# Optimization experiments

Hardware: AMD Instinct MI355X
Metric: run time of the kernel (lower is better)

## Reference

```python
import jax, jax.numpy as jnp
import numpy as np

DIM = 1024
HEADS = 16
DIM_K = DIM // HEADS
B, S = 2, 2048


def setup_inputs() -> dict:
    key = jax.random.key(0)
    ks = jax.random.split(key, 8)
    scale = 1.0 / np.sqrt(DIM)
    Q = jax.random.normal(ks[0], (B, S, DIM), dtype=jnp.float32)
    K = jax.random.normal(ks[1], (B, S, DIM), dtype=jnp.float32)
    V = jax.random.normal(ks[2], (B, S, DIM), dtype=jnp.float32)
    # causal mask, broadcastable [1,1,S,S]; masked_fill where mask == 0
    mask = jnp.tril(jnp.ones((S, S), dtype=bool))[None, None, :, :]
    wq = jax.random.normal(ks[3], (DIM, DIM), dtype=jnp.float32) * scale
    wk = jax.random.normal(ks[4], (DIM, DIM), dtype=jnp.float32) * scale
    wv = jax.random.normal(ks[5], (DIM, DIM), dtype=jnp.float32) * scale
    wo_w = jax.random.normal(ks[6], (DIM, DIM), dtype=jnp.float32) * scale
    wo_b = jnp.zeros((DIM,), dtype=jnp.float32)
    return {"Q": Q, "K": K, "V": V, "mask": mask,
            "wq": wq, "wk": wk, "wv": wv, "wo_w": wo_w, "wo_b": wo_b}


def reference(Q, K, V, mask, wq, wk, wv, wo_w, wo_b):
    b, s, d = Q.shape
    n_k = K.shape[1]
    # nn.Linear(bias=False): x @ W^T
    q = (Q @ wq.T).reshape(b, s, HEADS, DIM_K).transpose(0, 2, 1, 3)    # [b,h,s,dk]
    k = (K @ wk.T).reshape(b, n_k, HEADS, DIM_K).transpose(0, 2, 1, 3)  # [b,h,nk,dk]
    v = (V @ wv.T).reshape(b, n_k, HEADS, DIM_K).transpose(0, 2, 1, 3)
    inv_sqrt_dk = 1.0 / np.sqrt(DIM_K).astype(np.float32)
    scores = jnp.einsum('bhsd,bhtd->bhst', q, k) * inv_sqrt_dk          # [b,h,s,nk]
    scores = jnp.where(mask, scores, jnp.float32(-1e9))
    weights = jax.nn.softmax(scores, axis=-1)  # dropout p=0 -> identity
    out = jnp.einsum('bhst,bhtd->bhsd', weights, v)
    out = out.transpose(0, 2, 1, 3).reshape(b, s, d)
    return out @ wo_w.T + wo_b
```

## Files before the change

kernel.cpp:

```cpp
#include <hip/hip_runtime.h>

#define DIMN 1024
#define HEADS 16
#define DK 64
#define BATCH 2
#define SEQ 2048
#define MROWS (BATCH*SEQ)

typedef __bf16 bf16x8 __attribute__((ext_vector_type(8)));
typedef float f32x4 __attribute__((ext_vector_type(4)));

__device__ __forceinline__ unsigned short f2bf(float f) {
    unsigned int u = __float_as_uint(f);
    u += 0x7FFFu + ((u >> 16) & 1u);
    return (unsigned short)(u >> 16);
}

__device__ __forceinline__ f32x4 mfma16(bf16x8 a, bf16x8 b, f32x4 c) {
    return __builtin_amdgcn_mfma_f32_16x16x32_bf16(a, b, c, 0, 0, 0);
}

__device__ __forceinline__ void gload_lds16(const void* g, void* l) {
    __builtin_amdgcn_global_load_lds(
        (const __attribute__((address_space(1))) unsigned int*)g,
        (__attribute__((address_space(3))) unsigned int*)l, 16, 0, 0);
}

__device__ __forceinline__ unsigned cvtpk_bf16(float lo, float hi) {
    unsigned r;
    asm("v_cvt_pk_bf16_f32 %0, %1, %2" : "=v"(r) : "v"(lo), "v"(hi));
    return r;
}

__global__ __launch_bounds__(256) void cvt_all_kernel(
    const float* __restrict__ s0, const float* __restrict__ s1, const float* __restrict__ s2,
    const float* __restrict__ s3, const float* __restrict__ s4, const float* __restrict__ s5,
    const float* __restrict__ s6,
    unsigned short* __restrict__ d0, unsigned short* __restrict__ d1,
    unsigned short* __restrict__ d2, unsigned short* __restrict__ d3,
    unsigned short* __restrict__ d4, unsigned short* __restrict__ d5,
    unsigned short* __restrict__ d6) {
    int bb = blockIdx.x;
    const float* src; unsigned short* dst; int base;
    if (bb < 12288) {
        int w = bb >> 12; base = bb & 4095;
        src = (w == 0) ? s0 : (w == 1) ? s1 : s2;
        dst = (w == 0) ? d0 : (w == 1) ? d1 : d2;
    } else {
        int w = (bb - 12288) >> 10; base = bb & 1023;
        src = (w == 0) ? s3 : (w == 1) ? s4 : (w == 2) ? s5 : s6;
        dst = (w == 0) ? d3 : (w == 1) ? d4 : (w == 2) ? d5 : d6;
    }
    int i = (base * 256 + threadIdx.x) * 4;
    float4 v = *reinterpret_cast<const float4*>(src + i);
    ushort4 o;
    o.x = f2bf(v.x); o.y = f2bf(v.y); o.z = f2bf(v.z); o.w = f2bf(v.w);
    *reinterpret_cast<ushort4*>(dst + i) = o;
}

template<int BMM, bool OUT_F32, bool BIAS, typename CT>
__device__ __forceinline__ void gemm_core(
    const unsigned short* __restrict__ A, const unsigned short* __restrict__ W,
    CT* __restrict__ Cv, const float* __restrict__ bias, float oscale,
    unsigned short (&Asm)[2][BMM * 32], unsigned short (&Bsm)[2][128 * 32]) {
    const int tid = threadIdx.x, wid = tid >> 6, lane = tid & 63;
    const int m0 = blockIdx.x * BMM, n0 = blockIdx.y * 128;
    constexpr int MR = BMM / 32;
    const int wr = (wid >> 1) * (BMM / 2), wc = (wid & 1) * 64;
    const int lrow = lane & 15, lko = (lane >> 4) * 8;

    f32x4 acc[MR][4];
#pragma unroll
    for (int m = 0; m < MR; m++)
#pragma unroll
        for (int n = 0; n < 4; n++) acc[m][n] = f32x4{0.f, 0.f, 0.f, 0.f};

    const int offA = wid * 1024 + lane * 16;
    auto stage = [&](int buf, int k0) {
#pragma unroll
        for (int j = 0; j < BMM / 64; j++) {
            int off = j * 4096 + offA;
            int row = off >> 6, colb = off & 63;
            gload_lds16(A + (size_t)(m0 + row) * DIMN + k0 + (colb >> 1),
                        &Asm[buf][(j * 4096 + wid * 1024) >> 1]);
        }
#pragma unroll
        for (int j = 0; j < 2; j++) {
            int off = j * 4096 + offA;
            int row = off >> 6, colb = off & 63;
            gload_lds16(W + (size_t)(n0 + row) * DIMN + k0 + (colb >> 1),
                        &Bsm[buf][(j * 4096 + wid * 1024) >> 1]);
        }
    };

    stage(0, 0);
    __syncthreads();
    const int nk = DIMN / 32;
    int cur = 0;
    for (int t = 0; t < nk; t++) {
        if (t + 1 < nk) stage(cur ^ 1, (t + 1) * 32);
        bf16x8 af[MR], bfr[4];
#pragma unroll
        for (int m = 0; m < MR; m++)
            af[m] = *(const bf16x8*)&Asm[cur][(wr + m * 16 + lrow) * 32 + lko];
#pragma unroll
        for (int n = 0; n < 4; n++)
            bfr[n] = *(const bf16x8*)&Bsm[cur][(wc + n * 16 + lrow) * 32 + lko];
#pragma unroll
        for (int m = 0; m < MR; m++)
#pragma unroll
            for (int n = 0; n < 4; n++)
                acc[m][n] = mfma16(af[m], bfr[n], acc[m][n]);
        __syncthreads();
        cur ^= 1;
    }

    const int rbase = (lane >> 4) * 4;
    const int cbase = lane & 15;
#pragma unroll
    for (int m = 0; m < MR; m++) {
#pragma unroll
        for (int n = 0; n < 4; n++) {
#pragma unroll
            for (int r = 0; r < 4; r++) {
                int row = m0 + wr + m * 16 + rbase + r;
                int col = n0 + wc + n * 16 + cbase;
                float v = acc[m][n][r] * oscale;
                if (BIAS) v += bias[col];
                if (OUT_F32)
                    ((float*)Cv)[(size_t)row * DIMN + col] = v;
                else
                    ((unsigned short*)Cv)[(size_t)row * DIMN + col] = f2bf(v);
            }
        }
    }
}

__global__ __launch_bounds__(256, 2) void gemm_proj3_kernel(
    const unsigned short* __restrict__ A0, const unsigned short* __restrict__ A1,
    const unsigned short* __restrict__ A2,
    const unsigned short* __restrict__ W0, const unsigned short* __restrict__ W1,
    const unsigned short* __restrict__ W2,
    unsigned short* __restrict__ C0, unsigned short* __restrict__ C1,
    unsigned short* __restrict__ C2) {
    __shared__ unsigned short Asm[2][128 * 32];
    __shared__ unsigned short Bsm[2][128 * 32];
    const int z = blockIdx.z;
    const unsigned short* A = (z == 0) ? A0 : (z == 1) ? A1 : A2;
    const unsigned short* W = (z == 0) ? W0 : (z == 1) ? W1 : W2;
    unsigned short* C = (z == 0) ? C0 : (z == 1) ? C1 : C2;
    const float os = (z == 0) ? 0.18033688011112042f : 1.0f;
    gemm_core<128, false, false>(A, W, C, (const float*)nullptr, os, Asm, Bsm);
}

__global__ __launch_bounds__(256, 2) void gemm_out_kernel(
    const unsigned short* __restrict__ A, const unsigned short* __restrict__ W,
    float* __restrict__ C, const float* __restrict__ bias) {
    __shared__ unsigned short Asm[2][64 * 32];
    __shared__ unsigned short Bsm[2][128 * 32];
    gemm_core<64, true, true>(A, W, C, bias, 1.0f, Asm, Bsm);
}

__global__ __launch_bounds__(256) void vtrans_kernel(
    const unsigned short* __restrict__ vp, unsigned short* __restrict__ vt) {
    const int r0 = blockIdx.x * 64;
    const int h = blockIdx.y;
    const int b = r0 >> 11;
    const int s0 = r0 & 2047;
    __shared__ unsigned short T[64][72];
    const int tid = threadIdx.x;
#pragma unroll
    for (int jj = 0; jj < 2; jj++) {
        int idx = tid + 256 * jj;
        int row = idx >> 3, ch = idx & 7;
        uint4 v = *(const uint4*)(vp + (size_t)(r0 + row) * DIMN + h * DK + ch * 8);
        *(uint4*)&T[row][ch * 8] = v;
    }
    __syncthreads();
#pragma unroll
    for (int jj = 0; jj < 4; jj++) {
        int cid = tid + 256 * jj;
        int d = cid >> 4, rem = cid & 15;
        int G = rem >> 3, g = (rem >> 1) & 3, t = rem & 1;
        int sl = G * 32 + 16 * t + 4 * g;
        ushort4 o;
        o.x = T[sl + 0][d]; o.y = T[sl + 1][d]; o.z = T[sl + 2][d]; o.w = T[sl + 3][d];
        size_t orow = (size_t)((b * HEADS + h) * 64 + d);
        *(ushort4*)(vt + orow * SEQ + s0 + G * 32 + g * 8 + t * 4) = o;
    }
}

template<bool DIAG>
__device__ __forceinline__ void attn_tile(
    const unsigned short* __restrict__ Kc, const unsigned short* __restrict__ Vc,
    bf16x8 qf0, bf16x8 qf1, f32x4 (&o)[4], float& lrun,
    const int c, const int g, const int k0, const int qq) {
    float p[16];
    float rs = 0.f;
#pragma unroll
    for (int t = 0; t < 4; t++) {
        const int row = t * 16 + c;
        bf16x8 ka0 = *(const bf16x8*)&Kc[row * 64 + ((g ^ (c & 7)) * 8)];
        bf16x8 ka1 = *(const bf16x8*)&Kc[row * 64 + (((4 + g) ^ (c & 7)) * 8)];
        f32x4 s = mfma16(ka0, qf0, f32x4{0.f, 0.f, 0.f, 0.f});
        s = mfma16(ka1, qf1, s);
        const int kbase = k0 + t * 16 + 4 * g;
#pragma unroll
        for (int r = 0; r < 4; r++) {
            float pe = __builtin_exp2f(s[r]);
            if (DIAG && (kbase + r) > qq) pe = 0.f;
            p[t * 4 + r] = pe;
            rs += pe;
        }
    }
    rs += __shfl_xor(rs, 16);
    rs += __shfl_xor(rs, 32);
    lrun += rs;

    unsigned pk[8];
#pragma unroll
    for (int t = 0; t < 4; t++) {
        pk[t * 2 + 0] = cvtpk_bf16(p[t * 4 + 0], p[t * 4 + 1]);
        pk[t * 2 + 1] = cvtpk_bf16(p[t * 4 + 2], p[t * 4 + 3]);
    }
#pragma unroll
    for (int ks = 0; ks < 2; ks++) {
        union { unsigned u[4]; bf16x8 v; } pa;
        pa.u[0] = pk[4 * ks + 0]; pa.u[1] = pk[4 * ks + 1];
        pa.u[2] = pk[4 * ks + 2]; pa.u[3] = pk[4 * ks + 3];
#pragma unroll
        for (int dt = 0; dt < 4; dt++) {
            const int row = dt * 16 + c;
            bf16x8 vb = *(const bf16x8*)&Vc[row * 64 + ((((ks * 4) + g) ^ (c & 7)) * 8)];
            o[dt] = mfma16(pa.v, vb, o[dt]);
        }
    }
}

__global__ __launch_bounds__(256, 2) void attn_kernel(
    const unsigned short* __restrict__ qp, const unsigned short* __restrict__ kp,
    const unsigned short* __restrict__ vt, unsigned short* __restrict__ ao) {
    const int tid = threadIdx.x, wid = tid >> 6, lane = tid & 63;
    const int c = lane & 15, g = lane >> 4;
    const int blk = blockIdx.x;
    const int kk = blk >> 3;
    const int bh = (blk & 7) + 8 * (kk >> 4);
    const int j = kk & 15;
    const int qA = j * 64;
    const int qB = (31 - j) * 64;
    const int b = bh >> 4, h = bh & 15;

    __shared__ unsigned short Kt[2][64 * 64];
    __shared__ unsigned short Vt[2][64 * 64];

    const unsigned short* qrowA = qp + (size_t)(b * SEQ + qA + wid * 16 + c) * DIMN + h * DK;
    bf16x8 qfA0 = *(const bf16x8*)(qrowA + g * 8);
    bf16x8 qfA1 = *(const bf16x8*)(qrowA + 32 + g * 8);
    const unsigned short* qrowB = qp + (size_t)(b * SEQ + qB + wid * 16 + c) * DIMN + h * DK;
    bf16x8 qfB0 = *(const bf16x8*)(qrowB + g * 8);
    bf16x8 qfB1 = *(const bf16x8*)(qrowB + 32 + g * 8);

    f32x4 oA[4], oB[4];
#pragma unroll
    for (int dt = 0; dt < 4; dt++) {
        oA[dt] = f32x4{0.f, 0.f, 0.f, 0.f};
        oB[dt] = f32x4{0.f, 0.f, 0.f, 0.f};
    }
    float lrunA = 0.f, lrunB = 0.f;

    const int nktB = 32 - j;
    const int qqA = qA + wid * 16 + c;
    const int qqB = qB + wid * 16 + c;

    auto stage = [&](int buf, int k0) {
#pragma unroll
        for (int jj = 0; jj < 2; jj++) {
            int boff = (jj * 4 + wid) * 1024;
            int off = boff + lane * 16;
            int row = off >> 7;
            int sch = ((off >> 4) & 7) ^ (row & 7);
            gload_lds16(kp + (size_t)(b * SEQ + k0 + row) * DIMN + h * DK + sch * 8,
                        (char*)&Kt[buf][0] + boff);
            gload_lds16(vt + (size_t)(bh * 64 + row) * SEQ + k0 + sch * 8,
                        (char*)&Vt[buf][0] + boff);
        }
    };

    stage(0, 0);
    __syncthreads();
    int cur = 0;
    for (int kt = 0; kt < nktB; kt++) {
        if (kt + 1 < nktB) stage(cur ^ 1, (kt + 1) * 64);
        const int k0 = kt * 64;
        const unsigned short* Kc = &Kt[cur][0];
        const unsigned short* Vc = &Vt[cur][0];

        if (kt == nktB - 1)
            attn_tile<true>(Kc, Vc, qfB0, qfB1, oB, lrunB, c, g, k0, qqB);
        else
            attn_tile<false>(Kc, Vc, qfB0, qfB1, oB, lrunB, c, g, k0, qqB);

        if (kt < j)
            attn_tile<false>(Kc, Vc, qfA0, qfA1, oA, lrunA, c, g, k0, qqA);
        else if (kt == j)
            attn_tile<true>(Kc, Vc, qfA0, qfA1, oA, lrunA, c, g, k0, qqA);

        __syncthreads();
        cur ^= 1;
    }

    float lrA[4], lrB[4];
#pragma unroll
    for (int r = 0; r < 4; r++) {
        lrA[r] = 1.0f / __shfl(lrunA, 4 * g + r);
        lrB[r] = 1.0f / __shfl(lrunB, 4 * g + r);
    }
#pragma unroll
    for (int dt = 0; dt < 4; dt++)
#pragma unroll
        for (int r = 0; r < 4; r++) {
            ao[(size_t)(b * SEQ + qA + wid * 16 + 4 * g + r) * DIMN + h * DK + dt * 16 + c] =
                f2bf(oA[dt][r] * lrA[r]);
            ao[(size_t)(b * SEQ + qB + wid * 16 + 4 * g + r) * DIMN + h * DK + dt * 16 + c] =
                f2bf(oB[dt][r] * lrB[r]);
        }
}

extern "C" void kernel_launch(void* const* d_in, const int* in_sizes, int n_in,
                              void* d_out, int out_size, void* d_ws, size_t ws_size,
                              hipStream_t stream) {
    const float* Q  = (const float*)d_in[0];
    const float* K  = (const float*)d_in[1];
    const float* V  = (const float*)d_in[2];
    const float* wq = (const float*)d_in[4];
    const float* wk = (const float*)d_in[5];
    const float* wv = (const float*)d_in[6];
    const float* wo = (const float*)d_in[7];
    const float* wob = (const float*)d_in[8];

    char* ws = (char*)d_ws;
    const size_t SZ_ACT = (size_t)MROWS * DIMN * 2;
    const size_t SZ_W   = (size_t)DIMN * DIMN * 2;
    unsigned short* Qb  = (unsigned short*)(ws);
    unsigned short* Kb  = (unsigned short*)(ws + SZ_ACT);
    unsigned short* Vb  = (unsigned short*)(ws + 2 * SZ_ACT);
    unsigned short* Wqb = (unsigned short*)(ws + 3 * SZ_ACT);
    unsigned short* Wkb = (unsigned short*)(ws + 3 * SZ_ACT + SZ_W);
    unsigned short* Wvb = (unsigned short*)(ws + 3 * SZ_ACT + 2 * SZ_W);
    unsigned short* Wob = (unsigned short*)(ws + 3 * SZ_ACT + 3 * SZ_W);
    unsigned short* qp  = (unsigned short*)(ws + 3 * SZ_ACT + 4 * SZ_W);
    unsigned short* kp  = (unsigned short*)(ws + 4 * SZ_ACT + 4 * SZ_W);
    unsigned short* vp  = (unsigned short*)(ws + 5 * SZ_ACT + 4 * SZ_W);
    unsigned short* vt  = Vb;
    unsigned short* aob = Qb;

    cvt_all_kernel<<<16384, 256, 0, stream>>>(Q, K, V, wq, wk, wv, wo,
                                              Qb, Kb, Vb, Wqb, Wkb, Wvb, Wob);

    dim3 gp(MROWS / 128, DIMN / 128, 3);
    gemm_proj3_kernel<<<gp, 256, 0, stream>>>(Qb, Kb, Vb, Wqb, Wkb, Wvb, qp, kp, vp);

    dim3 gt(MROWS / 64, HEADS);
    vtrans_kernel<<<gt, 256, 0, stream>>>(vp, vt);

    attn_kernel<<<512, 256, 0, stream>>>(qp, kp, vt, aob);

    dim3 go(MROWS / 64, DIMN / 128);
    gemm_out_kernel<<<go, 256, 0, stream>>>(aob, Wob, (float*)d_out, wob);
}
```

Measured before the change: 133.7 us.

## Fuse fp32-to-bf16 activation conversion into projection GEMM and swizzle LDS tiles

The Q/K/V inputs are no longer converted to bf16 in a separate pass. The projection GEMM now loads fp32 tiles straight into LDS and converts them to bf16 with v_cvt_pk_bf16_f32 just before the MFMA. This removes a full read and write of the 48 MB of activations, though the GEMM now pulls twice the A bytes per tile and uses more LDS. XOR swizzling is also added to the LDS layouts of A and B to cut bank conflicts on fragment reads.

```diff
diff --git a/kernel.cpp b/kernel.cpp
--- a/kernel.cpp
+++ b/kernel.cpp
@@ -32,25 +32,15 @@
     return r;
 }
 
-__global__ __launch_bounds__(256) void cvt_all_kernel(
-    const float* __restrict__ s0, const float* __restrict__ s1, const float* __restrict__ s2,
-    const float* __restrict__ s3, const float* __restrict__ s4, const float* __restrict__ s5,
-    const float* __restrict__ s6,
+__global__ __launch_bounds__(256) void cvt_w_kernel(
+    const float* __restrict__ s0, const float* __restrict__ s1,
+    const float* __restrict__ s2, const float* __restrict__ s3,
     unsigned short* __restrict__ d0, unsigned short* __restrict__ d1,
-    unsigned short* __restrict__ d2, unsigned short* __restrict__ d3,
-    unsigned short* __restrict__ d4, unsigned short* __restrict__ d5,
-    unsigned short* __restrict__ d6) {
+    unsigned short* __restrict__ d2, unsigned short* __restrict__ d3) {
     int bb = blockIdx.x;
-    const float* src; unsigned short* dst; int base;
-    if (bb < 12288) {
-        int w = bb >> 12; base = bb & 4095;
-        src = (w == 0) ? s0 : (w == 1) ? s1 : s2;
-        dst = (w == 0) ? d0 : (w == 1) ? d1 : d2;
-    } else {
-        int w = (bb - 12288) >> 10; base = bb & 1023;
-        src = (w == 0) ? s3 : (w == 1) ? s4 : (w == 2) ? s5 : s6;
-        dst = (w == 0) ? d3 : (w == 1) ? d4 : (w == 2) ? d5 : d6;
-    }
+    int w = bb >> 10, base = bb & 1023;
+    const float* src = (w == 0) ? s0 : (w == 1) ? s1 : (w == 2) ? s2 : s3;
+    unsigned short* dst = (w == 0) ? d0 : (w == 1) ? d1 : (w == 2) ? d2 : d3;
     int i = (base * 256 + threadIdx.x) * 4;
     float4 v = *reinterpret_cast<const float4*>(src + i);
     ushort4 o;
@@ -58,16 +48,16 @@
     *reinterpret_cast<ushort4*>(dst + i) = o;
 }
 
-template<int BMM, bool OUT_F32, bool BIAS, typename CT>
+template<int BMM, bool AF32, bool OUT_F32, bool BIAS>
 __device__ __forceinline__ void gemm_core(
-    const unsigned short* __restrict__ A, const unsigned short* __restrict__ W,
-    CT* __restrict__ Cv, const float* __restrict__ bias, float oscale,
-    unsigned short (&Asm)[2][BMM * 32], unsigned short (&Bsm)[2][128 * 32]) {
+    const void* __restrict__ Av, const unsigned short* __restrict__ W,
+    void* __restrict__ Cv, const float* __restrict__ bias, float oscale,
+    void* __restrict__ AsmV, unsigned short (&Bsm)[2][128 * 32]) {
     const int tid = threadIdx.x, wid = tid >> 6, lane = tid & 63;
     const int m0 = blockIdx.x * BMM, n0 = blockIdx.y * 128;
     constexpr int MR = BMM / 32;
     const int wr = (wid >> 1) * (BMM / 2), wc = (wid & 1) * 64;
-    const int lrow = lane & 15, lko = (lane >> 4) * 8;
+    const int lrow = lane & 15, g = lane >> 4;
 
     f32x4 acc[MR][4];
 #pragma unroll
@@ -75,37 +65,74 @@
 #pragma unroll
         for (int n = 0; n < 4; n++) acc[m][n] = f32x4{0.f, 0.f, 0.f, 0.f};
 
-    const int offA = wid * 1024 + lane * 16;
-    auto stage = [&](int buf, int k0) {
-#pragma unroll
-        for (int j = 0; j < BMM / 64; j++) {
-            int off = j * 4096 + offA;
-            int row = off >> 6, colb = off & 63;
-            gload_lds16(A + (size_t)(m0 + row) * DIMN + k0 + (colb >> 1),
-                        &Asm[buf][(j * 4096 + wid * 1024) >> 1]);
-        }
-#pragma unroll
-        for (int j = 0; j < 2; j++) {
-            int off = j * 4096 + offA;
-            int row = off >> 6, colb = off & 63;
-            gload_lds16(W + (size_t)(n0 + row) * DIMN + k0 + (colb >> 1),
-                        &Bsm[buf][(j * 4096 + wid * 1024) >> 1]);
+    auto stageA = [&](int buf, int k0) {
+        if constexpr (AF32) {
+            const float* Af = (const float*)Av;
+#pragma unroll
+            for (int jj = 0; jj < BMM / 32; jj++) {
+                int off = jj * 4096 + wid * 1024 + lane * 16;
+                int row = off >> 7;
+                int sch = ((off >> 4) & 7) ^ (row & 7);
+                gload_lds16(Af + (size_t)(m0 + row) * DIMN + k0 + sch * 4,
+                            (char*)AsmV + buf * (BMM * 128) + jj * 4096 + wid * 1024);
+            }
+        } else {
+            const unsigned short* Ab = (const unsigned short*)Av;
+#pragma unroll
+            for (int jj = 0; jj < BMM / 64; jj++) {
+                int off = jj * 4096 + wid * 1024 + lane * 16;
+                int row = off >> 6;
+                int sch = ((off >> 4) & 3) ^ ((row >> 1) & 3);
+                gload_lds16(Ab + (size_t)(m0 + row) * DIMN + k0 + sch * 8,
+                            (char*)AsmV + buf * (BMM * 64) + jj * 4096 + wid * 1024);
+            }
         }
     };
-
-    stage(0, 0);
+    auto stageB = [&](int buf, int k0) {
+#pragma unroll
+        for (int jj = 0; jj < 2; jj++) {
+            int off = jj * 4096 + wid * 1024 + lane * 16;
+            int row = off >> 6;
+            int sch = ((off >> 4) & 3) ^ ((row >> 1) & 3);
+            gload_lds16(W + (size_t)(n0 + row) * DIMN + k0 + sch * 8,
+                        (char*)&Bsm[buf][0] + jj * 4096 + wid * 1024);
+        }
+    };
+
+    stageA(0, 0); stageB(0, 0);
     __syncthreads();
-    const int nk = DIMN / 32;
     int cur = 0;
-    for (int t = 0; t < nk; t++) {
-        if (t + 1 < nk) stage(cur ^ 1, (t + 1) * 32);
+    for (int t = 0; t < 32; t++) {
+        if (t + 1 < 32) { stageA(cur ^ 1, (t + 1) * 32); stageB(cur ^ 1, (t + 1) * 32); }
         bf16x8 af[MR], bfr[4];
-#pragma unroll
-        for (int m = 0; m < MR; m++)
-            af[m] = *(const bf16x8*)&Asm[cur][(wr + m * 16 + lrow) * 32 + lko];
-#pragma unroll
-        for (int n = 0; n < 4; n++)
-            bfr[n] = *(const bf16x8*)&Bsm[cur][(wc + n * 16 + lrow) * 32 + lko];
+        if constexpr (AF32) {
+            const float* Asm = (const float*)AsmV + cur * (BMM * 32);
+#pragma unroll
+            for (int m = 0; m < MR; m++) {
+                int row = wr + m * 16 + lrow;
+                int c0 = (2 * g) ^ (row & 7), c1 = (2 * g + 1) ^ (row & 7);
+                f32x4 lo = *(const f32x4*)&Asm[row * 32 + c0 * 4];
+                f32x4 hi = *(const f32x4*)&Asm[row * 32 + c1 * 4];
+                union { unsigned u[4]; bf16x8 v; } a;
+                a.u[0] = cvtpk_bf16(lo[0], lo[1]); a.u[1] = cvtpk_bf16(lo[2], lo[3]);
+                a.u[2] = cvtpk_bf16(hi[0], hi[1]); a.u[3] = cvtpk_bf16(hi[2], hi[3]);
+                af[m] = a.v;
+            }
+        } else {
+            const unsigned short* Asm = (const unsigned short*)AsmV + cur * (BMM * 32);
+#pragma unroll
+            for (int m = 0; m < MR; m++) {
+                int row = wr + m * 16 + lrow;
+                int ch = g ^ ((row >> 1) & 3);
+                af[m] = *(const bf16x8*)&Asm[row * 32 + ch * 8];
+            }
+        }
+#pragma unroll
+        for (int n = 0; n < 4; n++) {
+            int row = wc + n * 16 + lrow;
+            int ch = g ^ ((row >> 1) & 3);
+            bfr[n] = *(const bf16x8*)&Bsm[cur][row * 32 + ch * 8];
+        }
 #pragma unroll
         for (int m = 0; m < MR; m++)
 #pragma unroll
@@ -115,8 +142,7 @@
         cur ^= 1;
     }
 
-    const int rbase = (lane >> 4) * 4;
-    const int cbase = lane & 15;
+    const int rbase = g * 4;
 #pragma unroll
     for (int m = 0; m < MR; m++) {
 #pragma unroll
@@ -124,7 +150,7 @@
 #pragma unroll
             for (int r = 0; r < 4; r++) {
                 int row = m0 + wr + m * 16 + rbase + r;
-                int col = n0 + wc + n * 16 + cbase;
+                int col = n0 + wc + n * 16 + lrow;
                 float v = acc[m][n][r] * oscale;
                 if (BIAS) v += bias[col];
                 if (OUT_F32)
@@ -137,28 +163,28 @@
 }
 
 __global__ __launch_bounds__(256, 2) void gemm_proj3_kernel(
-    const unsigned short* __restrict__ A0, const unsigned short* __restrict__ A1,
-    const unsigned short* __restrict__ A2,
+    const float* __restrict__ A0, const float* __restrict__ A1,
+    const float* __restrict__ A2,
     const unsigned short* __restrict__ W0, const unsigned short* __restrict__ W1,
     const unsigned short* __restrict__ W2,
     unsigned short* __restrict__ C0, unsigned short* __restrict__ C1,
     unsigned short* __restrict__ C2) {
-    __shared__ unsigned short Asm[2][128 * 32];
+    __shared__ float AsmF[2][128 * 32];
     __shared__ unsigned short Bsm[2][128 * 32];
     const int z = blockIdx.z;
-    const unsigned short* A = (z == 0) ? A0 : (z == 1) ? A1 : A2;
+    const float* A = (z == 0) ? A0 : (z == 1) ? A1 : A2;
     const unsigned short* W = (z == 0) ? W0 : (z == 1) ? W1 : W2;
     unsigned short* C = (z == 0) ? C0 : (z == 1) ? C1 : C2;
     const float os = (z == 0) ? 0.18033688011112042f : 1.0f;
-    gemm_core<128, false, false>(A, W, C, (const float*)nullptr, os, Asm, Bsm);
+    gemm_core<128, true, false, false>(A, W, C, (const float*)nullptr, os, AsmF, Bsm);
 }
 
 __global__ __launch_bounds__(256, 2) void gemm_out_kernel(
     const unsigned short* __restrict__ A, const unsigned short* __restrict__ W,
     float* __restrict__ C, const float* __restrict__ bias) {
-    __shared__ unsigned short Asm[2][64 * 32];
+    __shared__ unsigned short AsmH[2][64 * 32];
     __shared__ unsigned short Bsm[2][128 * 32];
-    gemm_core<64, true, true>(A, W, C, bias, 1.0f, Asm, Bsm);
+    gemm_core<64, false, true, true>(A, W, C, bias, 1.0f, AsmH, Bsm);
 }
 
 __global__ __launch_bounds__(256) void vtrans_kernel(
@@ -341,29 +367,25 @@
     char* ws = (char*)d_ws;
     const size_t SZ_ACT = (size_t)MROWS * DIMN * 2;
     const size_t SZ_W   = (size_t)DIMN * DIMN * 2;
-    unsigned short* Qb  = (unsigned short*)(ws);
-    unsigned short* Kb  = (unsigned short*)(ws + SZ_ACT);
-    unsigned short* Vb  = (unsigned short*)(ws + 2 * SZ_ACT);
-    unsigned short* Wqb = (unsigned short*)(ws + 3 * SZ_ACT);
-    unsigned short* Wkb = (unsigned short*)(ws + 3 * SZ_ACT + SZ_W);
-    unsigned short* Wvb = (unsigned short*)(ws + 3 * SZ_ACT + 2 * SZ_W);
-    unsigned short* Wob = (unsigned short*)(ws + 3 * SZ_ACT + 3 * SZ_W);
-    unsigned short* qp  = (unsigned short*)(ws + 3 * SZ_ACT + 4 * SZ_W);
-    unsigned short* kp  = (unsigned short*)(ws + 4 * SZ_ACT + 4 * SZ_W);
-    unsigned short* vp  = (unsigned short*)(ws + 5 * SZ_ACT + 4 * SZ_W);
-    unsigned short* vt  = Vb;
-    unsigned short* aob = Qb;
-
-    cvt_all_kernel<<<16384, 256, 0, stream>>>(Q, K, V, wq, wk, wv, wo,
-                                              Qb, Kb, Vb, Wqb, Wkb, Wvb, Wob);
+    unsigned short* vtb = (unsigned short*)(ws);
+    unsigned short* aob = (unsigned short*)(ws + SZ_ACT);
+    unsigned short* Wqb = (unsigned short*)(ws + 2 * SZ_ACT);
+    unsigned short* Wkb = (unsigned short*)(ws + 2 * SZ_ACT + SZ_W);
+    unsigned short* Wvb = (unsigned short*)(ws + 2 * SZ_ACT + 2 * SZ_W);
+    unsigned short* Wob = (unsigned short*)(ws + 2 * SZ_ACT + 3 * SZ_W);
+    unsigned short* qp  = (unsigned short*)(ws + 2 * SZ_ACT + 4 * SZ_W);
+    unsigned short* kp  = (unsigned short*)(ws + 3 * SZ_ACT + 4 * SZ_W);
+    unsigned short* vp  = (unsigned short*)(ws + 4 * SZ_ACT + 4 * SZ_W);
+
+    cvt_w_kernel<<<4096, 256, 0, stream>>>(wq, wk, wv, wo, Wqb, Wkb, Wvb, Wob);
 
     dim3 gp(MROWS / 128, DIMN / 128, 3);
-    gemm_proj3_kernel<<<gp, 256, 0, stream>>>(Qb, Kb, Vb, Wqb, Wkb, Wvb, qp, kp, vp);
+    gemm_proj3_kernel<<<gp, 256, 0, stream>>>(Q, K, V, Wqb, Wkb, Wvb, qp, kp, vp);
 
     dim3 gt(MROWS / 64, HEADS);
-    vtrans_kernel<<<gt, 256, 0, stream>>>(vp, vt);
-
-    attn_kernel<<<512, 256, 0, stream>>>(qp, kp, vt, aob);
+    vtrans_kernel<<<gt, 256, 0, stream>>>(vp, vtb);
+
+    attn_kernel<<<512, 256, 0, stream>>>(qp, kp, vtb, aob);
 
     dim3 go(MROWS / 64, DIMN / 128);
     gemm_out_kernel<<<go, 256, 0, stream>>>(aob, Wob, (float*)d_out, wob);
```

After: 123.9 us. 7.4% less time.

## Swizzle GEMM LDS tiles, use explicit vmcnt waits, triple-buffer attention K/V

Applied to the files above, without the earlier changes.

The GEMM core now writes A and W tiles to LDS with an XOR swizzle on 16-byte chunks and reads them back with the matching swizzle, to avoid LDS bank conflicts on the fragment reads. Its loop replaces __syncthreads with explicit s_waitcnt vmcnt counts and raw s_barrier, so the next tile's async loads stay in flight while the current tile is computed. The attention kernel moves to a 3-stage K/V ring with a prefetch distance of two, and the projection GEMM's launch bounds go from 2 to 3 blocks. The hand-written vmcnt values assume a fixed number of outstanding loads per stage, so a wrong count could cause a race. The extra attention buffer also raises LDS use per block.

```diff
diff --git a/kernel.cpp b/kernel.cpp
--- a/kernel.cpp
+++ b/kernel.cpp
@@ -58,16 +58,16 @@
     *reinterpret_cast<ushort4*>(dst + i) = o;
 }
 
-template<int BMM, bool OUT_F32, bool BIAS, typename CT>
+template<int BMM, bool OUT_F32, bool BIAS>
 __device__ __forceinline__ void gemm_core(
     const unsigned short* __restrict__ A, const unsigned short* __restrict__ W,
-    CT* __restrict__ Cv, const float* __restrict__ bias, float oscale,
+    void* __restrict__ Cv, const float* __restrict__ bias, float oscale,
     unsigned short (&Asm)[2][BMM * 32], unsigned short (&Bsm)[2][128 * 32]) {
     const int tid = threadIdx.x, wid = tid >> 6, lane = tid & 63;
     const int m0 = blockIdx.x * BMM, n0 = blockIdx.y * 128;
     constexpr int MR = BMM / 32;
     const int wr = (wid >> 1) * (BMM / 2), wc = (wid & 1) * 64;
-    const int lrow = lane & 15, lko = (lane >> 4) * 8;
+    const int lrow = lane & 15, g = lane >> 4;
 
     f32x4 acc[MR][4];
 #pragma unroll
@@ -75,48 +75,67 @@
 #pragma unroll
         for (int n = 0; n < 4; n++) acc[m][n] = f32x4{0.f, 0.f, 0.f, 0.f};
 
-    const int offA = wid * 1024 + lane * 16;
-    auto stage = [&](int buf, int k0) {
-#pragma unroll
-        for (int j = 0; j < BMM / 64; j++) {
-            int off = j * 4096 + offA;
-            int row = off >> 6, colb = off & 63;
-            gload_lds16(A + (size_t)(m0 + row) * DIMN + k0 + (colb >> 1),
-                        &Asm[buf][(j * 4096 + wid * 1024) >> 1]);
-        }
-#pragma unroll
-        for (int j = 0; j < 2; j++) {
-            int off = j * 4096 + offA;
-            int row = off >> 6, colb = off & 63;
-            gload_lds16(W + (size_t)(n0 + row) * DIMN + k0 + (colb >> 1),
-                        &Bsm[buf][(j * 4096 + wid * 1024) >> 1]);
+    auto stageA = [&](int buf, int k0) {
+#pragma unroll
+        for (int jj = 0; jj < BMM / 64; jj++) {
+            int off = jj * 4096 + wid * 1024 + lane * 16;
+            int row = off >> 6;
+            int sch = ((off >> 4) & 3) ^ ((row >> 1) & 3);
+            gload_lds16(A + (size_t)(m0 + row) * DIMN + k0 + sch * 8,
+                        (char*)&Asm[buf][0] + jj * 4096 + wid * 1024);
         }
     };
-
-    stage(0, 0);
-    __syncthreads();
-    const int nk = DIMN / 32;
+    auto stageB = [&](int buf, int k0) {
+#pragma unroll
+        for (int jj = 0; jj < 2; jj++) {
+            int off = jj * 4096 + wid * 1024 + lane * 16;
+            int row = off >> 6;
+            int sch = ((off >> 4) & 3) ^ ((row >> 1) & 3);
+            gload_lds16(W + (size_t)(n0 + row) * DIMN + k0 + sch * 8,
+                        (char*)&Bsm[buf][0] + jj * 4096 + wid * 1024);
+        }
+    };
+
+    stageA(0, 0); stageB(0, 0);
     int cur = 0;
-    for (int t = 0; t < nk; t++) {
-        if (t + 1 < nk) stage(cur ^ 1, (t + 1) * 32);
+    for (int t = 0; t < 32; t++) {
+        if (t + 1 < 32) {
+            stageA(cur ^ 1, (t + 1) * 32); stageB(cur ^ 1, (t + 1) * 32);
+            if constexpr ((BMM / 64 + 2) == 3)
+                asm volatile("s_waitcnt vmcnt(3)" ::: "memory");
+            else
+                asm volatile("s_waitcnt vmcnt(4)" ::: "memory");
+        } else {
+            asm volatile("s_waitcnt vmcnt(0)" ::: "memory");
+        }
+        __builtin_amdgcn_s_barrier();
+        __builtin_amdgcn_sched_barrier(0);
+
         bf16x8 af[MR], bfr[4];
 #pragma unroll
-        for (int m = 0; m < MR; m++)
-            af[m] = *(const bf16x8*)&Asm[cur][(wr + m * 16 + lrow) * 32 + lko];
-#pragma unroll
-        for (int n = 0; n < 4; n++)
-            bfr[n] = *(const bf16x8*)&Bsm[cur][(wc + n * 16 + lrow) * 32 + lko];
+        for (int m = 0; m < MR; m++) {
+            int row = wr + m * 16 + lrow;
+            int ch = g ^ ((row >> 1) & 3);
+            af[m] = *(const bf16x8*)&Asm[cur][row * 32 + ch * 8];
+        }
+#pragma unroll
+        for (int n = 0; n < 4; n++) {
+            int row = wc + n * 16 + lrow;
+            int ch = g ^ ((row >> 1) & 3);
+            bfr[n] = *(const bf16x8*)&Bsm[cur][row * 32 + ch * 8];
+        }
 #pragma unroll
         for (int m = 0; m < MR; m++)
 #pragma unroll
             for (int n = 0; n < 4; n++)
                 acc[m][n] = mfma16(af[m], bfr[n], acc[m][n]);
-        __syncthreads();
+
+        __builtin_amdgcn_sched_barrier(0);
+        __builtin_amdgcn_s_barrier();
         cur ^= 1;
     }
 
-    const int rbase = (lane >> 4) * 4;
-    const int cbase = lane & 15;
+    const int rbase = g * 4;
 #pragma unroll
     for (int m = 0; m < MR; m++) {
 #pragma unroll
@@ -124,7 +143,7 @@
 #pragma unroll
             for (int r = 0; r < 4; r++) {
                 int row = m0 + wr + m * 16 + rbase + r;
-                int col = n0 + wc + n * 16 + cbase;
+                int col = n0 + wc + n * 16 + lrow;
                 float v = acc[m][n][r] * oscale;
                 if (BIAS) v += bias[col];
                 if (OUT_F32)
@@ -136,7 +155,7 @@
     }
 }
 
-__global__ __launch_bounds__(256, 2) void gemm_proj3_kernel(
+__global__ __launch_bounds__(256, 3) void gemm_proj3_kernel(
     const unsigned short* __restrict__ A0, const unsigned short* __restrict__ A1,
     const unsigned short* __restrict__ A2,
     const unsigned short* __restrict__ W0, const unsigned short* __restrict__ W1,
@@ -156,9 +175,9 @@
 __global__ __launch_bounds__(256, 2) void gemm_out_kernel(
     const unsigned short* __restrict__ A, const unsigned short* __restrict__ W,
     float* __restrict__ C, const float* __restrict__ bias) {
-    __shared__ unsigned short Asm[2][64 * 32];
+    __shared__ unsigned short AsmH[2][64 * 32];
     __shared__ unsigned short Bsm[2][128 * 32];
-    gemm_core<64, true, true>(A, W, C, bias, 1.0f, Asm, Bsm);
+    gemm_core<64, true, true>(A, W, C, bias, 1.0f, AsmH, Bsm);
 }
 
 __global__ __launch_bounds__(256) void vtrans_kernel(
@@ -250,8 +269,8 @@
     const int qB = (31 - j) * 64;
     const int b = bh >> 4, h = bh & 15;
 
-    __shared__ unsigned short Kt[2][64 * 64];
-    __shared__ unsigned short Vt[2][64 * 64];
+    __shared__ unsigned short Kt[3][64 * 64];
+    __shared__ unsigned short Vt[3][64 * 64];
 
     const unsigned short* qrowA = qp + (size_t)(b * SEQ + qA + wid * 16 + c) * DIMN + h * DK;
     bf16x8 qfA0 = *(const bf16x8*)(qrowA + g * 8);
@@ -287,10 +306,20 @@
     };
 
     stage(0, 0);
-    __syncthreads();
-    int cur = 0;
+    stage(1, 64);
     for (int kt = 0; kt < nktB; kt++) {
-        if (kt + 1 < nktB) stage(cur ^ 1, (kt + 1) * 64);
+        if (kt + 2 < nktB) {
+            stage((kt + 2) % 3, (kt + 2) * 64);
+            asm volatile("s_waitcnt vmcnt(8)" ::: "memory");
+        } else if (kt + 1 < nktB) {
+            asm volatile("s_waitcnt vmcnt(4)" ::: "memory");
+        } else {
+            asm volatile("s_waitcnt vmcnt(0)" ::: "memory");
+        }
+        __builtin_amdgcn_s_barrier();
+        __builtin_amdgcn_sched_barrier(0);
+
+        const int cur = kt % 3;
         const int k0 = kt * 64;
         const unsigned short* Kc = &Kt[cur][0];
         const unsigned short* Vc = &Vt[cur][0];
@@ -305,8 +334,8 @@
         else if (kt == j)
             attn_tile<true>(Kc, Vc, qfA0, qfA1, oA, lrunA, c, g, k0, qqA);
 
-        __syncthreads();
-        cur ^= 1;
+        __builtin_amdgcn_sched_barrier(0);
+        __builtin_amdgcn_s_barrier();
     }
 
     float lrA[4], lrB[4];
```

After: 127.6 us. 4.6% less time.
